# Kernel tuning notes

Hardware: AMD Instinct MI355X
Metric: run time of the kernel (lower is better)

## Reference

```python
import jax, jax.numpy as jnp
import numpy as np

N, E, H, L = 50000, 400000, 100, 2
NF, EF = 16, 8
BN_EPS = 1e-5  # torch BatchNorm1d eps; eval mode with running_mean=0, running_var=1


def setup_inputs() -> dict:
    key = jax.random.key(0)
    ks = jax.random.split(key, 32)
    s = 0.05
    rn = lambda k, shape: jax.random.normal(k, shape, dtype=jnp.float32) * s
    return {
        "x": jax.random.normal(ks[0], (N, NF), dtype=jnp.float32),
        "edge_index": jax.random.randint(ks[1], (2, E), 0, N, dtype=jnp.int32),
        "edge_attr": jax.random.normal(ks[2], (E, EF), dtype=jnp.float32),
        "node_w": rn(ks[3], (NF, H)), "node_b": rn(ks[4], (H,)),
        "edge_w": rn(ks[5], (EF, H)), "edge_b": rn(ks[6], (H,)),
        "conv_w1": rn(ks[7], (L, H, H)), "conv_b1": rn(ks[8], (L, H)),
        "conv_w2": rn(ks[9], (L, H, H)), "conv_b2": rn(ks[10], (L, H)),
        "bn_gamma": jnp.ones((L, H), jnp.float32), "bn_beta": jnp.zeros((L, H), jnp.float32),
        "em_w1": rn(ks[11], (L, 3 * H, H)), "em_b1": rn(ks[12], (L, H)),
        "em_w2": rn(ks[13], (L, H, H)), "em_b2": rn(ks[14], (L, H)),
        "mlp_w1": rn(ks[15], (3 * H, 50)), "mlp_b1": rn(ks[16], (50,)),
        "mlp_w2": rn(ks[17], (50, 25)), "mlp_b2": rn(ks[18], (25,)),
        "mlp_w3": rn(ks[19], (25, 1)), "mlp_b3": rn(ks[20], (1,)),
    }


def reference(x, edge_index, edge_attr, node_w, node_b, edge_w, edge_b,
              conv_w1, conv_b1, conv_w2, conv_b2, bn_gamma, bn_beta,
              em_w1, em_b1, em_w2, em_b2,
              mlp_w1, mlp_b1, mlp_w2, mlp_b2, mlp_w3, mlp_b3):
    src, dst = edge_index[0], edge_index[1]
    h = x @ node_w + node_b            # [N,H]
    e = edge_attr @ edge_w + edge_b    # [E,H]
    bn_inv = 1.0 / jnp.sqrt(1.0 + BN_EPS)
    for i in range(L):
        # GINEConv (eps=0): MLP(x + sum_{j->i} relu(x_j + e_ji))
        msg = jax.nn.relu(h[src] + e)                                  # [E,H]
        agg = jax.ops.segment_sum(msg, dst, num_segments=h.shape[0])   # [N,H]
        z = h + agg
        z = jax.nn.relu(z @ conv_w1[i] + conv_b1[i]) @ conv_w2[i] + conv_b2[i]
        bn = z * (bn_gamma[i] * bn_inv) + bn_beta[i]                   # BN eval (mean 0, var 1)
        h = (h + jax.nn.relu(bn)) * 0.5
        ei = jnp.concatenate([h[src], h[dst], e], axis=-1)             # [E,3H]
        e = e + (jax.nn.relu(ei @ em_w1[i] + em_b1[i]) @ em_w2[i] + em_b2[i]) * 0.5
    xe = jnp.concatenate([h[src], h[dst], e], axis=-1)                 # [E,3H]
    o = jax.nn.relu(xe @ mlp_w1 + mlp_b1)
    o = jax.nn.relu(o @ mlp_w2 + mlp_b2)
    return (o @ mlp_w3 + mlp_b3)[:, 0]                                 # [E]
```

## Files before the change

### kernel.cpp

```cpp
#include <hip/hip_runtime.h>

#define HD 100
#define NF 16
#define EF 8
#define NN 50000
#define NE 400000
#define NT64 6250

typedef __attribute__((ext_vector_type(8))) short bf16x8;
typedef __attribute__((ext_vector_type(4))) float f32x4;

__device__ __forceinline__ float frelu(float v) { return v > 0.f ? v : 0.f; }
__device__ __forceinline__ unsigned short f2bf(float f) {
  unsigned int u = __float_as_uint(f);
  unsigned int r = (u + 0x7FFF + ((u >> 16) & 1)) >> 16;
  return (unsigned short)r;
}
__device__ __forceinline__ int SWZ(int row, int byte) { return byte ^ ((row & 7) << 4); }
__device__ __forceinline__ float4 L4(const float* p) { return *(const float4*)p; }
__device__ __forceinline__ uint2 bf2x4(float4 f, float4 g) {
  uint2 o;
  o.x = (unsigned)f2bf(f.x) | ((unsigned)f2bf(f.y) << 16);
  o.y = (unsigned)f2bf(f.z) | ((unsigned)f2bf(f.w) << 16);
  (void)g;
  return o;
}

__global__ __launch_bounds__(256) void k_pack(const float* __restrict__ W,
    unsigned short* __restrict__ out, int K, int N, int KS, int NT) {
  int t = blockIdx.x * 256 + threadIdx.x;
  if (t >= KS * NT * 64) return;
  int lane = t & 63, nt = (t >> 6) % NT, ks = (t >> 6) / NT;
  int kb = ks * 32 + (lane >> 4) * 8, n = nt * 16 + (lane & 15);
  unsigned short v[8];
  #pragma unroll
  for (int j = 0; j < 8; ++j) {
    int k = kb + j;
    float f = (k < K && n < N) ? W[(size_t)k * N + n] : 0.f;
    v[j] = f2bf(f);
  }
  uint4 o4;
  o4.x = (unsigned)v[0] | ((unsigned)v[1] << 16);
  o4.y = (unsigned)v[2] | ((unsigned)v[3] << 16);
  o4.z = (unsigned)v[4] | ((unsigned)v[5] << 16);
  o4.w = (unsigned)v[6] | ((unsigned)v[7] << 16);
  *(uint4*)&out[(size_t)t * 8] = o4;
}

__global__ __launch_bounds__(256) void k_node_embed(const float* __restrict__ x,
    const float* __restrict__ w, const float* __restrict__ b, float* __restrict__ h) {
  int t = blockIdx.x * 256 + threadIdx.x;
  int n = t / HD, o = t % HD;
  if (n >= NN) return;
  float acc = b[o];
  #pragma unroll
  for (int k = 0; k < NF; ++k) acc = fmaf(x[n * NF + k], w[k * HD + o], acc);
  h[(size_t)n * HD + o] = acc;
}

__global__ __launch_bounds__(256) void k_edge_embed_perm(const float* __restrict__ ea,
    const int* __restrict__ eids, const float* __restrict__ w, const float* __restrict__ b,
    float* __restrict__ e) {
  __shared__ float ws_[EF * HD];
  __shared__ float bs_[HD];
  int tid = threadIdx.x;
  for (int i = tid; i < EF * HD; i += 256) ws_[i] = w[i];
  for (int i = tid; i < HD; i += 256) bs_[i] = b[i];
  __syncthreads();
  long long t = (long long)blockIdx.x * 256 + tid;
  int p = (int)(t / 25), c4 = (int)(t % 25);
  if (p >= NE) return;
  int eid = eids[p];
  const float* ap = ea + (size_t)eid * EF;
  float4 a0 = L4(ap), a1 = L4(ap + 4);
  float av[8] = {a0.x, a0.y, a0.z, a0.w, a1.x, a1.y, a1.z, a1.w};
  int c0 = c4 * 4;
  float o0 = bs_[c0], o1 = bs_[c0 + 1], o2 = bs_[c0 + 2], o3 = bs_[c0 + 3];
  #pragma unroll
  for (int k = 0; k < EF; ++k) {
    const float* wr = &ws_[k * HD + c0];
    o0 = fmaf(av[k], wr[0], o0); o1 = fmaf(av[k], wr[1], o1);
    o2 = fmaf(av[k], wr[2], o2); o3 = fmaf(av[k], wr[3], o3);
  }
  float4 o; o.x = o0; o.y = o1; o.z = o2; o.w = o3;
  ((float4*)e)[(size_t)p * 25 + c4] = o;
}

__global__ __launch_bounds__(256) void k_hist(const int* __restrict__ dst, int* __restrict__ deg) {
  int eid = blockIdx.x * 256 + threadIdx.x;
  if (eid < NE) atomicAdd(&deg[dst[eid]], 1);
}
__global__ __launch_bounds__(256) void k_scan_part(const int* __restrict__ deg, int* __restrict__ part) {
  __shared__ int sm[256];
  int i = blockIdx.x * 256 + threadIdx.x;
  sm[threadIdx.x] = (i < NN) ? deg[i] : 0;
  __syncthreads();
  for (int s = 128; s > 0; s >>= 1) {
    if (threadIdx.x < s) sm[threadIdx.x] += sm[threadIdx.x + s];
    __syncthreads();
  }
  if (threadIdx.x == 0) part[blockIdx.x] = sm[0];
}
__global__ __launch_bounds__(256) void k_scan_top(int* __restrict__ part, int nb) {
  __shared__ int sm[256];
  int v = (threadIdx.x < nb) ? part[threadIdx.x] : 0;
  sm[threadIdx.x] = v;
  __syncthreads();
  for (int off = 1; off < 256; off <<= 1) {
    int t = (threadIdx.x >= (unsigned)off) ? sm[threadIdx.x - off] : 0;
    __syncthreads();
    sm[threadIdx.x] += t;
    __syncthreads();
  }
  if (threadIdx.x < nb) part[threadIdx.x] = sm[threadIdx.x] - v;
}
__global__ __launch_bounds__(256) void k_scan_fill(const int* __restrict__ deg,
    const int* __restrict__ part, int* __restrict__ rowptr) {
  __shared__ int sm[256];
  int i = blockIdx.x * 256 + threadIdx.x;
  int v = (i < NN) ? deg[i] : 0;
  sm[threadIdx.x] = v;
  __syncthreads();
  for (int off = 1; off < 256; off <<= 1) {
    int t = (threadIdx.x >= (unsigned)off) ? sm[threadIdx.x - off] : 0;
    __syncthreads();
    sm[threadIdx.x] += t;
    __syncthreads();
  }
  if (i <= NN) rowptr[i] = part[blockIdx.x] + sm[threadIdx.x] - v;
}
__global__ __launch_bounds__(256) void k_copy(const int* __restrict__ a, int* __restrict__ b) {
  int i = blockIdx.x * 256 + threadIdx.x;
  if (i < NN) b[i] = a[i];
}
__global__ __launch_bounds__(256) void k_fill(const int* __restrict__ dst,
    int* __restrict__ cursor, int* __restrict__ eids) {
  int eid = blockIdx.x * 256 + threadIdx.x;
  if (eid >= NE) return;
  int pos = atomicAdd(&cursor[dst[eid]], 1);
  eids[pos] = eid;
}

__global__ __launch_bounds__(256) void k_gather(const float* __restrict__ h,
    const float* __restrict__ e, const int* __restrict__ rowptr,
    const int* __restrict__ eids, const int* __restrict__ src, float* __restrict__ agg) {
  int slot = threadIdx.x >> 2, sub = threadIdx.x & 3;
  int n = blockIdx.x * 64 + slot;
  if (n >= NN) return;
  int r0 = rowptr[n], r1 = rowptr[n + 1];
  float4 acc[7];
  #pragma unroll
  for (int i = 0; i < 7; ++i) { acc[i].x = 0.f; acc[i].y = 0.f; acc[i].z = 0.f; acc[i].w = 0.f; }
  for (int p = r0; p < r1; ++p) {
    int s = src[eids[p]];
    const float4* hp = (const float4*)&h[(size_t)s * HD];
    const float4* ep = (const float4*)&e[(size_t)p * HD];
    #pragma unroll
    for (int i = 0; i < 7; ++i) {
      int c = sub + i * 4;
      if (c < 25) {
        float4 hv = hp[c], ev = ep[c];
        acc[i].x += frelu(hv.x + ev.x);
        acc[i].y += frelu(hv.y + ev.y);
        acc[i].z += frelu(hv.z + ev.z);
        acc[i].w += frelu(hv.w + ev.w);
      }
    }
  }
  float4* ap = (float4*)&agg[(size_t)n * HD];
  #pragma unroll
  for (int i = 0; i < 7; ++i) {
    int c = sub + i * 4;
    if (c < 25) ap[c] = acc[i];
  }
}

__global__ __launch_bounds__(256) void k_node_update(float* __restrict__ h,
    const float* __restrict__ agg,
    const float* __restrict__ w1, const float* __restrict__ b1,
    const float* __restrict__ w2, const float* __restrict__ b2,
    const float* __restrict__ gamma, const float* __restrict__ beta) {
  __shared__ float zs[64 * 101];
  int tid = threadIdx.x;
  int base = blockIdx.x * 64;
  for (int idx = tid; idx < 64 * HD; idx += 256) {
    int n = idx / HD, k = idx % HD;
    int gn = base + n; int cn = gn < NN ? gn : NN - 1;
    zs[n * 101 + k] = h[(size_t)cn * HD + k] + agg[(size_t)cn * HD + k];
  }
  __syncthreads();
  int el = tid & 63;
  int o0 = __builtin_amdgcn_readfirstlane((tid >> 6) * 25);
  float* row = &zs[el * 101];
  float acc[25];
  #pragma unroll
  for (int j = 0; j < 25; ++j) acc[j] = b1[o0 + j];
  for (int k = 0; k < HD; ++k) {
    float a = row[k];
    const float* wr = &w1[k * HD + o0];
    #pragma unroll
    for (int j = 0; j < 25; ++j) acc[j] = fmaf(a, wr[j], acc[j]);
  }
  __syncthreads();
  #pragma unroll
  for (int j = 0; j < 25; ++j) row[o0 + j] = frelu(acc[j]);
  __syncthreads();
  float acc2[25];
  #pragma unroll
  for (int j = 0; j < 25; ++j) acc2[j] = b2[o0 + j];
  for (int k = 0; k < HD; ++k) {
    float a = row[k];
    const float* wr = &w2[k * HD + o0];
    #pragma unroll
    for (int j = 0; j < 25; ++j) acc2[j] = fmaf(a, wr[j], acc2[j]);
  }
  int gn = base + el;
  if (gn < NN) {
    const float bninv = 0.99999500003749973f;
    #pragma unroll
    for (int j = 0; j < 25; ++j) {
      int o = o0 + j;
      float bn = acc2[j] * (gamma[o] * bninv) + beta[o];
      h[(size_t)gn * HD + o] = (h[(size_t)gn * HD + o] + frelu(bn)) * 0.5f;
    }
  }
}

__global__ __launch_bounds__(512) void k_edge_mfma(
    const float* __restrict__ h, float* __restrict__ e,
    const int* __restrict__ eids, const int* __restrict__ src, const int* __restrict__ dst,
    const unsigned short* __restrict__ w1p, const float* __restrict__ b1,
    const unsigned short* __restrict__ w2p, const float* __restrict__ b2) {
  __shared__ __align__(16) char lds[151040];
  char* W1L = lds;
  char* W2L = lds + 64512;
  char* A1  = lds + 93184;
  char* A2  = lds + 134144;
  int* ss  = (int*)(lds + 150528);
  int* ds_ = (int*)(lds + 150784);
  int tid = threadIdx.x;
  for (int i = tid; i < 4032; i += 512) ((uint4*)W1L)[i] = ((const uint4*)w1p)[i];
  for (int i = tid; i < 1792; i += 512) ((uint4*)W2L)[i] = ((const uint4*)w2p)[i];

  int lane = tid & 63, w = tid >> 6;
  int l15 = lane & 15, lq = lane >> 4;
  int g = w >> 2;
  int arow = (w & 3) * 16 + l15;
  int ntb = g * 4, ntc = g ? 3 : 4;
  f32x4 zero = {0.f, 0.f, 0.f, 0.f};

  for (int tile = blockIdx.x; tile < NT64; tile += gridDim.x) {
    int base = tile * 64;
    if (tid < 64) { int eid = eids[base + tid]; ss[tid] = src[eid]; ds_[tid] = dst[eid]; }
    __syncthreads();
    for (int idx = tid; idx < 64 * 25; idx += 512) {
      int row = idx / 25, c4 = idx % 25;
      float4 f = ((const float4*)e)[(size_t)(base + row) * 25 + c4];
      *(uint2*)(A1 + SWZ(row, row * 640 + 400 + c4 * 8)) = bf2x4(f, f);
    }
    for (int idx = tid; idx < 64 * 25; idx += 512) {
      int row = idx / 25, c4 = idx % 25;
      float4 f = ((const float4*)h)[(size_t)ss[row] * 25 + c4];
      *(uint2*)(A1 + SWZ(row, row * 640 + c4 * 8)) = bf2x4(f, f);
    }
    for (int idx = tid; idx < 64 * 25; idx += 512) {
      int row = idx / 25, c4 = idx % 25;
      float4 f = ((const float4*)h)[(size_t)ds_[row] * 25 + c4];
      *(uint2*)(A1 + SWZ(row, row * 640 + 200 + c4 * 8)) = bf2x4(f, f);
    }
    for (int idx = tid; idx < 64 * 5; idx += 512) {
      int row = idx / 5, j = idx % 5;
      uint2 z; z.x = 0u; z.y = 0u;
      *(uint2*)(A1 + SWZ(row, row * 640 + 600 + j * 8)) = z;
    }
    __syncthreads();
    f32x4 acc[4];
    #pragma unroll
    for (int i = 0; i < 4; ++i) acc[i] = zero;
    #pragma unroll
    for (int ks = 0; ks < 10; ++ks) {
      bf16x8 a = *(const bf16x8*)(A1 + SWZ(arow, arow * 640 + (ks * 32 + lq * 8) * 2));
      #pragma unroll
      for (int i = 0; i < 4; ++i) {
        if (i < ntc) {
          int nt = ntb + i;
          bf16x8 b = (ks < 9)
            ? *(const bf16x8*)(W1L + ks * 7168 + (nt * 64 + lane) * 16)
            : *(const bf16x8*)(w1p + (size_t)9 * 3584 + (nt * 64 + lane) * 8);
          acc[i] = __builtin_amdgcn_mfma_f32_16x16x32_bf16(a, b, acc[i], 0, 0, 0);
        }
      }
    }
    #pragma unroll
    for (int i = 0; i < 4; ++i) {
      if (i < ntc) {
        int o = (ntb + i) * 16 + l15;
        float bias = (o < HD) ? b1[o] : 0.f;
        #pragma unroll
        for (int ii = 0; ii < 4; ++ii) {
          int r = (w & 3) * 16 + lq * 4 + ii;
          float v = acc[i][ii] + bias;
          v = (o < HD) ? frelu(v) : 0.f;
          *(unsigned short*)(A2 + SWZ(r, r * 256 + o * 2)) = f2bf(v);
        }
      }
    }
    for (int idx = tid; idx < 64 * 8; idx += 512) {
      int r = idx / 8, c = idx % 8;
      *(unsigned int*)(A2 + SWZ(r, r * 256 + 224 + c * 4)) = 0;
    }
    __syncthreads();
    f32x4 acc2[4];
    #pragma unroll
    for (int i = 0; i < 4; ++i) acc2[i] = zero;
    #pragma unroll
    for (int ks = 0; ks < 4; ++ks) {
      bf16x8 a = *(const bf16x8*)(A2 + SWZ(arow, arow * 256 + (ks * 32 + lq * 8) * 2));
      #pragma unroll
      for (int i = 0; i < 4; ++i) {
        if (i < ntc) {
          int nt = ntb + i;
          bf16x8 b = *(const bf16x8*)(W2L + ks * 7168 + (nt * 64 + lane) * 16);
          acc2[i] = __builtin_amdgcn_mfma_f32_16x16x32_bf16(a, b, acc2[i], 0, 0, 0);
        }
      }
    }
    #pragma unroll
    for (int i = 0; i < 4; ++i) {
      if (i < ntc) {
        int o = (ntb + i) * 16 + l15;
        if (o < HD) {
          float bias = b2[o];
          #pragma unroll
          for (int ii = 0; ii < 4; ++ii) {
            int r = (w & 3) * 16 + lq * 4 + ii;
            size_t pp = (size_t)(base + r) * HD + o;
            e[pp] = e[pp] + 0.5f * (acc2[i][ii] + bias);
          }
        }
      }
    }
    __syncthreads();
  }
}

__global__ __launch_bounds__(512) void k_edge_final_mfma(
    const float* __restrict__ h, const float* __restrict__ e,
    const int* __restrict__ eids, const int* __restrict__ src, const int* __restrict__ dst,
    const unsigned short* __restrict__ w1p, const float* __restrict__ b1,
    const unsigned short* __restrict__ w2p, const float* __restrict__ b2,
    const unsigned short* __restrict__ wf1p, const float* __restrict__ fb1,
    const float* __restrict__ fw2, const float* __restrict__ fb2,
    const float* __restrict__ fw3, const float* __restrict__ fb3,
    float* __restrict__ out) {
  __shared__ __align__(16) char lds[156500];
  char* W1L = lds;
  char* W2L = lds + 64512;
  char* A1  = lds + 93184;
  char* A2  = lds + 134144;
  float* W2s = (float*)(lds + 150528);
  float* b2s = (float*)(lds + 155528);
  float* W3s = (float*)(lds + 155628);
  float* b3s = (float*)(lds + 155728);
  int* es  = (int*)(lds + 155732);
  int* ss  = (int*)(lds + 155988);
  int* ds_ = (int*)(lds + 156244);
  int tid = threadIdx.x;
  for (int i = tid; i < 4032; i += 512) ((uint4*)W1L)[i] = ((const uint4*)w1p)[i];
  for (int i = tid; i < 1792; i += 512) ((uint4*)W2L)[i] = ((const uint4*)w2p)[i];
  for (int i = tid; i < 1250; i += 512) W2s[i] = fw2[i];
  if (tid < 25) { b2s[tid] = fb2[tid]; W3s[tid] = fw3[tid]; }
  if (tid == 0) b3s[0] = fb3[0];

  int lane = tid & 63, w = tid >> 6;
  int l15 = lane & 15, lq = lane >> 4;
  int g = w >> 2;
  int arow = (w & 3) * 16 + l15;
  int ntb = g * 4, ntc = g ? 3 : 4;
  f32x4 zero = {0.f, 0.f, 0.f, 0.f};

  for (int tile = blockIdx.x; tile < NT64; tile += gridDim.x) {
    int base = tile * 64;
    if (tid < 64) {
      int eid = eids[base + tid];
      es[tid] = eid; ss[tid] = src[eid]; ds_[tid] = dst[eid];
    }
    __syncthreads();
    for (int idx = tid; idx < 64 * 25; idx += 512) {
      int row = idx / 25, c4 = idx % 25;
      float4 f = ((const float4*)e)[(size_t)(base + row) * 25 + c4];
      *(uint2*)(A1 + SWZ(row, row * 640 + 400 + c4 * 8)) = bf2x4(f, f);
    }
    for (int idx = tid; idx < 64 * 25; idx += 512) {
      int row = idx / 25, c4 = idx % 25;
      float4 f = ((const float4*)h)[(size_t)ss[row] * 25 + c4];
      *(uint2*)(A1 + SWZ(row, row * 640 + c4 * 8)) = bf2x4(f, f);
    }
    for (int idx = tid; idx < 64 * 25; idx += 512) {
      int row = idx / 25, c4 = idx % 25;
      float4 f = ((const float4*)h)[(size_t)ds_[row] * 25 + c4];
      *(uint2*)(A1 + SWZ(row, row * 640 + 200 + c4 * 8)) = bf2x4(f, f);
    }
    for (int idx = tid; idx < 64 * 5; idx += 512) {
      int row = idx / 5, j = idx % 5;
      uint2 z; z.x = 0u; z.y = 0u;
      *(uint2*)(A1 + SWZ(row, row * 640 + 600 + j * 8)) = z;
    }
    __syncthreads();
    f32x4 acc[4];
    #pragma unroll
    for (int i = 0; i < 4; ++i) acc[i] = zero;
    #pragma unroll
    for (int ks = 0; ks < 10; ++ks) {
      bf16x8 a = *(const bf16x8*)(A1 + SWZ(arow, arow * 640 + (ks * 32 + lq * 8) * 2));
      #pragma unroll
      for (int i = 0; i < 4; ++i) {
        if (i < ntc) {
          int nt = ntb + i;
          bf16x8 b = (ks < 9)
            ? *(const bf16x8*)(W1L + ks * 7168 + (nt * 64 + lane) * 16)
            : *(const bf16x8*)(w1p + (size_t)9 * 3584 + (nt * 64 + lane) * 8);
          acc[i] = __builtin_amdgcn_mfma_f32_16x16x32_bf16(a, b, acc[i], 0, 0, 0);
        }
      }
    }
    #pragma unroll
    for (int i = 0; i < 4; ++i) {
      if (i < ntc) {
        int o = (ntb + i) * 16 + l15;
        float bias = (o < HD) ? b1[o] : 0.f;
        #pragma unroll
        for (int ii = 0; ii < 4; ++ii) {
          int r = (w & 3) * 16 + lq * 4 + ii;
          float v = acc[i][ii] + bias;
          v = (o < HD) ? frelu(v) : 0.f;
          *(unsigned short*)(A2 + SWZ(r, r * 256 + o * 2)) = f2bf(v);
        }
      }
    }
    for (int idx = tid; idx < 64 * 8; idx += 512) {
      int r = idx / 8, c = idx % 8;
      *(unsigned int*)(A2 + SWZ(r, r * 256 + 224 + c * 4)) = 0;
    }
    __syncthreads();
    f32x4 acc2[4];
    #pragma unroll
    for (int i = 0; i < 4; ++i) acc2[i] = zero;
    #pragma unroll
    for (int ks = 0; ks < 4; ++ks) {
      bf16x8 a = *(const bf16x8*)(A2 + SWZ(arow, arow * 256 + (ks * 32 + lq * 8) * 2));
      #pragma unroll
      for (int i = 0; i < 4; ++i) {
        if (i < ntc) {
          int nt = ntb + i;
          bf16x8 b = *(const bf16x8*)(W2L + ks * 7168 + (nt * 64 + lane) * 16);
          acc2[i] = __builtin_amdgcn_mfma_f32_16x16x32_bf16(a, b, acc2[i], 0, 0, 0);
        }
      }
    }
    #pragma unroll
    for (int i = 0; i < 4; ++i) {
      if (i < ntc) {
        int o = (ntb + i) * 16 + l15;
        if (o < HD) {
          float bias = b2[o];
          #pragma unroll
          for (int ii = 0; ii < 4; ++ii) {
            int r = (w & 3) * 16 + lq * 4 + ii;
            float ne = e[(size_t)(base + r) * HD + o] + 0.5f * (acc2[i][ii] + bias);
            *(unsigned short*)(A1 + SWZ(r, r * 640 + (200 + o) * 2)) = f2bf(ne);
          }
        }
      }
    }
    __syncthreads();
    f32x4 acc3[2];
    acc3[0] = zero; acc3[1] = zero;
    #pragma unroll
    for (int ks = 0; ks < 10; ++ks) {
      bf16x8 a = *(const bf16x8*)(A1 + SWZ(arow, arow * 640 + (ks * 32 + lq * 8) * 2));
      #pragma unroll
      for (int i = 0; i < 2; ++i) {
        int nt = g * 2 + i;
        bf16x8 b = *(const bf16x8*)(wf1p + ((size_t)(ks * 4 + nt) * 64 + lane) * 8);
        acc3[i] = __builtin_amdgcn_mfma_f32_16x16x32_bf16(a, b, acc3[i], 0, 0, 0);
      }
    }
    __syncthreads();
    #pragma unroll
    for (int i = 0; i < 2; ++i) {
      int o = (g * 2 + i) * 16 + l15;
      if (o < 50) {
        float bias = fb1[o];
        #pragma unroll
        for (int ii = 0; ii < 4; ++ii) {
          int r = (w & 3) * 16 + lq * 4 + ii;
          *(float*)(A2 + r * 208 + o * 4) = frelu(acc3[i][ii] + bias);
        }
      }
    }
    __syncthreads();
    {
      int elg = tid >> 3, q8 = tid & 7;
      const float* trow = (const float*)(A2 + elg * 208);
      float s[4];
      {
        int i = 0;
        #pragma unroll
        for (int j0 = 0; j0 < 25; j0 += 8) { if (j0 + q8 < 25) s[i++] = b2s[j0 + q8]; }
      }
      for (int k = 0; k < 50; ++k) {
        float tv = trow[k];
        int i = 0;
        #pragma unroll
        for (int j0 = 0; j0 < 25; j0 += 8) {
          if (j0 + q8 < 25) { s[i] = fmaf(tv, W2s[k * 25 + j0 + q8], s[i]); ++i; }
        }
      }
      float racc = 0.f;
      {
        int i = 0;
        #pragma unroll
        for (int j0 = 0; j0 < 25; j0 += 8) {
          if (j0 + q8 < 25) { racc = fmaf(frelu(s[i]), W3s[j0 + q8], racc); ++i; }
        }
      }
      racc += __shfl_xor(racc, 1, 8);
      racc += __shfl_xor(racc, 2, 8);
      racc += __shfl_xor(racc, 4, 8);
      if (q8 == 0) out[es[elg]] = racc + b3s[0];
    }
    __syncthreads();
  }
}

extern "C" void kernel_launch(void* const* d_in, const int* in_sizes, int n_in,
                              void* d_out, int out_size, void* d_ws, size_t ws_size,
                              hipStream_t stream) {
  (void)in_sizes; (void)n_in; (void)out_size; (void)ws_size;
  const float* x       = (const float*)d_in[0];
  const int*   eidx    = (const int*)  d_in[1];
  const float* eattr   = (const float*)d_in[2];
  const float* node_w  = (const float*)d_in[3];
  const float* node_b  = (const float*)d_in[4];
  const float* edge_w  = (const float*)d_in[5];
  const float* edge_b  = (const float*)d_in[6];
  const float* conv_w1 = (const float*)d_in[7];
  const float* conv_b1 = (const float*)d_in[8];
  const float* conv_w2 = (const float*)d_in[9];
  const float* conv_b2 = (const float*)d_in[10];
  const float* bn_g    = (const float*)d_in[11];
  const float* bn_b    = (const float*)d_in[12];
  const float* em_w1   = (const float*)d_in[13];
  const float* em_b1   = (const float*)d_in[14];
  const float* em_w2   = (const float*)d_in[15];
  const float* em_b2   = (const float*)d_in[16];
  const float* mlp_w1  = (const float*)d_in[17];
  const float* mlp_b1  = (const float*)d_in[18];
  const float* mlp_w2  = (const float*)d_in[19];
  const float* mlp_b2  = (const float*)d_in[20];
  const float* mlp_w3  = (const float*)d_in[21];
  const float* mlp_b3  = (const float*)d_in[22];

  const int* src = eidx;
  const int* dst = eidx + NE;

  char* ws = (char*)d_ws;
  float* h    = (float*)(ws);
  float* agg  = (float*)(ws + 20000000);
  float* e    = (float*)(ws + 40000000);
  unsigned short* w1p  = (unsigned short*)(ws + 200000000);
  unsigned short* w2p  = (unsigned short*)(ws + 200071680);
  unsigned short* wf1p = (unsigned short*)(ws + 200100352);
  int* rowptr = (int*)(ws + 200141312);
  int* cursor = (int*)(ws + 200341504);
  int* eids   = (int*)(ws + 200541504);
  int* part   = (int*)(ws + 202141504);

  const int SCAN_NB = (NN + 256) / 256;
  hipMemsetAsync(cursor, 0, (size_t)NN * 4, stream);
  k_hist<<<(NE + 255) / 256, 256, 0, stream>>>(dst, cursor);
  k_scan_part<<<SCAN_NB, 256, 0, stream>>>(cursor, part);
  k_scan_top<<<1, 256, 0, stream>>>(part, SCAN_NB);
  k_scan_fill<<<SCAN_NB, 256, 0, stream>>>(cursor, part, rowptr);
  k_copy<<<SCAN_NB, 256, 0, stream>>>(rowptr, cursor);
  k_fill<<<(NE + 255) / 256, 256, 0, stream>>>(dst, cursor, eids);

  k_node_embed<<<(NN * HD + 255) / 256, 256, 0, stream>>>(x, node_w, node_b, h);
  {
    long long th = (long long)NE * 25;
    k_edge_embed_perm<<<(unsigned)((th + 255) / 256), 256, 0, stream>>>(eattr, eids, edge_w, edge_b, e);
  }

  k_pack<<<(10 * 4 * 64 + 255) / 256, 256, 0, stream>>>(mlp_w1, wf1p, 300, 50, 10, 4);

  for (int i = 0; i < 2; ++i) {
    k_gather<<<(NN + 63) / 64, 256, 0, stream>>>(h, e, rowptr, eids, src, agg);
    k_node_update<<<(NN + 63) / 64, 256, 0, stream>>>(
        h, agg, conv_w1 + i * HD * HD, conv_b1 + i * HD,
        conv_w2 + i * HD * HD, conv_b2 + i * HD, bn_g + i * HD, bn_b + i * HD);
    k_pack<<<(10 * 7 * 64 + 255) / 256, 256, 0, stream>>>(em_w1 + i * 30000, w1p, 300, 100, 10, 7);
    k_pack<<<(4 * 7 * 64 + 255) / 256, 256, 0, stream>>>(em_w2 + i * 10000,  w2p, 100, 100, 4, 7);
    if (i == 0) {
      k_edge_mfma<<<256, 512, 0, stream>>>(
          h, e, eids, src, dst, w1p, em_b1, w2p, em_b2);
    } else {
      k_edge_final_mfma<<<256, 512, 0, stream>>>(
          h, e, eids, src, dst, w1p, em_b1 + HD, w2p, em_b2 + HD,
          wf1p, mlp_b1, mlp_w2, mlp_b2, mlp_w3, mlp_b3, (float*)d_out);
    }
  }
}
```

Baseline: 885.1 us.

## Double-buffer edge tile staging to overlap gathers with MFMA compute

Both edge kernels now gather the next tile's h[src], h[dst] and e rows into a second LDS buffer while the current tile is being multiplied. This hides gather latency and removes a barrier per tile. To make room, W2 and the last two K-slices of W1 are now read from global memory instead of LDS, which adds global and L2 traffic inside the MFMA loops. In the final kernel, one barrier after the third GEMM is removed because A2 no longer aliases the buffer being read.

```diff
diff --git a/kernel.cpp b/kernel.cpp
--- a/kernel.cpp
+++ b/kernel.cpp
@@ -18,11 +18,10 @@
 }
 __device__ __forceinline__ int SWZ(int row, int byte) { return byte ^ ((row & 7) << 4); }
 __device__ __forceinline__ float4 L4(const float* p) { return *(const float4*)p; }
-__device__ __forceinline__ uint2 bf2x4(float4 f, float4 g) {
+__device__ __forceinline__ uint2 pk4(float4 f) {
   uint2 o;
   o.x = (unsigned)f2bf(f.x) | ((unsigned)f2bf(f.y) << 16);
   o.y = (unsigned)f2bf(f.z) | ((unsigned)f2bf(f.w) << 16);
-  (void)g;
   return o;
 }
 
@@ -226,21 +225,47 @@
   }
 }
 
+__device__ __forceinline__ void stage_tile(char* A1b, int tb, int tid,
+    const float* __restrict__ h, const float* __restrict__ e,
+    const int* __restrict__ eids, const int* __restrict__ src, const int* __restrict__ dst) {
+  int nbase = tb * 64;
+  for (int idx = tid; idx < 1600; idx += 512) {
+    int row = idx / 25, c4 = idx % 25;
+    float4 f = ((const float4*)e)[(size_t)(nbase + row) * 25 + c4];
+    *(uint2*)(A1b + SWZ(row, row * 640 + 400 + c4 * 8)) = pk4(f);
+  }
+  for (int idx = tid; idx < 1600; idx += 512) {
+    int row = idx / 25, c4 = idx % 25;
+    int s = src[eids[nbase + row]];
+    float4 f = ((const float4*)h)[(size_t)s * 25 + c4];
+    *(uint2*)(A1b + SWZ(row, row * 640 + c4 * 8)) = pk4(f);
+  }
+  for (int idx = tid; idx < 1600; idx += 512) {
+    int row = idx / 25, c4 = idx % 25;
+    int d = dst[eids[nbase + row]];
+    float4 f = ((const float4*)h)[(size_t)d * 25 + c4];
+    *(uint2*)(A1b + SWZ(row, row * 640 + 200 + c4 * 8)) = pk4(f);
+  }
+  if (tid < 320) {
+    int row = tid / 5, j = tid % 5;
+    uint2 z; z.x = 0u; z.y = 0u;
+    *(uint2*)(A1b + SWZ(row, row * 640 + 600 + j * 8)) = z;
+  }
+}
+
 __global__ __launch_bounds__(512) void k_edge_mfma(
     const float* __restrict__ h, float* __restrict__ e,
     const int* __restrict__ eids, const int* __restrict__ src, const int* __restrict__ dst,
     const unsigned short* __restrict__ w1p, const float* __restrict__ b1,
     const unsigned short* __restrict__ w2p, const float* __restrict__ b2) {
-  __shared__ __align__(16) char lds[151040];
+  __shared__ __align__(16) char lds[155648];
   char* W1L = lds;
-  char* W2L = lds + 64512;
-  char* A1  = lds + 93184;
-  char* A2  = lds + 134144;
-  int* ss  = (int*)(lds + 150528);
-  int* ds_ = (int*)(lds + 150784);
+  char* A1q = lds + 57344;
+  char* A2  = lds + 139264;
   int tid = threadIdx.x;
-  for (int i = tid; i < 4032; i += 512) ((uint4*)W1L)[i] = ((const uint4*)w1p)[i];
-  for (int i = tid; i < 1792; i += 512) ((uint4*)W2L)[i] = ((const uint4*)w2p)[i];
+  for (int i = tid; i < 3584; i += 512) ((uint4*)W1L)[i] = ((const uint4*)w1p)[i];
+  if (blockIdx.x < NT64) stage_tile(A1q, blockIdx.x, tid, h, e, eids, src, dst);
+  __syncthreads();
 
   int lane = tid & 63, w = tid >> 6;
   int l15 = lane & 15, lq = lane >> 4;
@@ -248,32 +273,14 @@
   int arow = (w & 3) * 16 + l15;
   int ntb = g * 4, ntc = g ? 3 : 4;
   f32x4 zero = {0.f, 0.f, 0.f, 0.f};
+  int cb = 0;
 
   for (int tile = blockIdx.x; tile < NT64; tile += gridDim.x) {
     int base = tile * 64;
-    if (tid < 64) { int eid = eids[base + tid]; ss[tid] = src[eid]; ds_[tid] = dst[eid]; }
-    __syncthreads();
-    for (int idx = tid; idx < 64 * 25; idx += 512) {
-      int row = idx / 25, c4 = idx % 25;
-      float4 f = ((const float4*)e)[(size_t)(base + row) * 25 + c4];
-      *(uint2*)(A1 + SWZ(row, row * 640 + 400 + c4 * 8)) = bf2x4(f, f);
-    }
-    for (int idx = tid; idx < 64 * 25; idx += 512) {
-      int row = idx / 25, c4 = idx % 25;
-      float4 f = ((const float4*)h)[(size_t)ss[row] * 25 + c4];
-      *(uint2*)(A1 + SWZ(row, row * 640 + c4 * 8)) = bf2x4(f, f);
-    }
-    for (int idx = tid; idx < 64 * 25; idx += 512) {
-      int row = idx / 25, c4 = idx % 25;
-      float4 f = ((const float4*)h)[(size_t)ds_[row] * 25 + c4];
-      *(uint2*)(A1 + SWZ(row, row * 640 + 200 + c4 * 8)) = bf2x4(f, f);
-    }
-    for (int idx = tid; idx < 64 * 5; idx += 512) {
-      int row = idx / 5, j = idx % 5;
-      uint2 z; z.x = 0u; z.y = 0u;
-      *(uint2*)(A1 + SWZ(row, row * 640 + 600 + j * 8)) = z;
-    }
-    __syncthreads();
+    char* A1 = A1q + cb * 40960;
+    int nxt = tile + gridDim.x;
+    if (nxt < NT64) stage_tile(A1q + (cb ^ 1) * 40960, nxt, tid, h, e, eids, src, dst);
+
     f32x4 acc[4];
     #pragma unroll
     for (int i = 0; i < 4; ++i) acc[i] = zero;
@@ -284,9 +291,9 @@
       for (int i = 0; i < 4; ++i) {
         if (i < ntc) {
           int nt = ntb + i;
-          bf16x8 b = (ks < 9)
+          bf16x8 b = (ks < 8)
             ? *(const bf16x8*)(W1L + ks * 7168 + (nt * 64 + lane) * 16)
-            : *(const bf16x8*)(w1p + (size_t)9 * 3584 + (nt * 64 + lane) * 8);
+            : *(const bf16x8*)(w1p + (size_t)ks * 3584 + (nt * 64 + lane) * 8);
           acc[i] = __builtin_amdgcn_mfma_f32_16x16x32_bf16(a, b, acc[i], 0, 0, 0);
         }
       }
@@ -305,10 +312,8 @@
         }
       }
     }
-    for (int idx = tid; idx < 64 * 8; idx += 512) {
-      int r = idx / 8, c = idx % 8;
-      *(unsigned int*)(A2 + SWZ(r, r * 256 + 224 + c * 4)) = 0;
-    }
+    { int r = tid / 8, c = tid % 8;
+      *(unsigned int*)(A2 + SWZ(r, r * 256 + 224 + c * 4)) = 0; }
     __syncthreads();
     f32x4 acc2[4];
     #pragma unroll
@@ -320,7 +325,7 @@
       for (int i = 0; i < 4; ++i) {
         if (i < ntc) {
           int nt = ntb + i;
-          bf16x8 b = *(const bf16x8*)(W2L + ks * 7168 + (nt * 64 + lane) * 16);
+          bf16x8 b = *(const bf16x8*)(w2p + ((size_t)(ks * 7 + nt) * 64 + lane) * 8);
           acc2[i] = __builtin_amdgcn_mfma_f32_16x16x32_bf16(a, b, acc2[i], 0, 0, 0);
         }
       }
@@ -341,6 +346,7 @@
       }
     }
     __syncthreads();
+    cb ^= 1;
   }
 }
 
@@ -353,24 +359,21 @@
     const float* __restrict__ fw2, const float* __restrict__ fb2,
     const float* __restrict__ fw3, const float* __restrict__ fb3,
     float* __restrict__ out) {
-  __shared__ __align__(16) char lds[156500];
+  __shared__ __align__(16) char lds[160856];
   char* W1L = lds;
-  char* W2L = lds + 64512;
-  char* A1  = lds + 93184;
-  char* A2  = lds + 134144;
-  float* W2s = (float*)(lds + 150528);
-  float* b2s = (float*)(lds + 155528);
-  float* W3s = (float*)(lds + 155628);
-  float* b3s = (float*)(lds + 155728);
-  int* es  = (int*)(lds + 155732);
-  int* ss  = (int*)(lds + 155988);
-  int* ds_ = (int*)(lds + 156244);
+  char* A1q = lds + 57344;
+  char* A2  = lds + 139264;
+  float* W2s = (float*)(lds + 155648);
+  float* b2s = (float*)(lds + 160648);
+  float* W3s = (float*)(lds + 160748);
+  float* b3s = (float*)(lds + 160848);
   int tid = threadIdx.x;
-  for (int i = tid; i < 4032; i += 512) ((uint4*)W1L)[i] = ((const uint4*)w1p)[i];
-  for (int i = tid; i < 1792; i += 512) ((uint4*)W2L)[i] = ((const uint4*)w2p)[i];
+  for (int i = tid; i < 3584; i += 512) ((uint4*)W1L)[i] = ((const uint4*)w1p)[i];
   for (int i = tid; i < 1250; i += 512) W2s[i] = fw2[i];
   if (tid < 25) { b2s[tid] = fb2[tid]; W3s[tid] = fw3[tid]; }
   if (tid == 0) b3s[0] = fb3[0];
+  if (blockIdx.x < NT64) stage_tile(A1q, blockIdx.x, tid, h, e, eids, src, dst);
+  __syncthreads();
 
   int lane = tid & 63, w = tid >> 6;
   int l15 = lane & 15, lq = lane >> 4;
@@ -378,35 +381,14 @@
   int arow = (w & 3) * 16 + l15;
   int ntb = g * 4, ntc = g ? 3 : 4;
   f32x4 zero = {0.f, 0.f, 0.f, 0.f};
+  int cb = 0;
 
   for (int tile = blockIdx.x; tile < NT64; tile += gridDim.x) {
     int base = tile * 64;
-    if (tid < 64) {
-      int eid = eids[base + tid];
-      es[tid] = eid; ss[tid] = src[eid]; ds_[tid] = dst[eid];
-    }
-    __syncthreads();
-    for (int idx = tid; idx < 64 * 25; idx += 512) {
-      int row = idx / 25, c4 = idx % 25;
-      float4 f = ((const float4*)e)[(size_t)(base + row) * 25 + c4];
-      *(uint2*)(A1 + SWZ(row, row * 640 + 400 + c4 * 8)) = bf2x4(f, f);
-    }
-    for (int idx = tid; idx < 64 * 25; idx += 512) {
-      int row = idx / 25, c4 = idx % 25;
-      float4 f = ((const float4*)h)[(size_t)ss[row] * 25 + c4];
-      *(uint2*)(A1 + SWZ(row, row * 640 + c4 * 8)) = bf2x4(f, f);
-    }
-    for (int idx = tid; idx < 64 * 25; idx += 512) {
-      int row = idx / 25, c4 = idx % 25;
-      float4 f = ((const float4*)h)[(size_t)ds_[row] * 25 + c4];
-      *(uint2*)(A1 + SWZ(row, row * 640 + 200 + c4 * 8)) = bf2x4(f, f);
-    }
-    for (int idx = tid; idx < 64 * 5; idx += 512) {
-      int row = idx / 5, j = idx % 5;
-      uint2 z; z.x = 0u; z.y = 0u;
-      *(uint2*)(A1 + SWZ(row, row * 640 + 600 + j * 8)) = z;
-    }
-    __syncthreads();
+    char* A1 = A1q + cb * 40960;
+    int nxt = tile + gridDim.x;
+    if (nxt < NT64) stage_tile(A1q + (cb ^ 1) * 40960, nxt, tid, h, e, eids, src, dst);
+
     f32x4 acc[4];
     #pragma unroll
     for (int i = 0; i < 4; ++i) acc[i] = zero;
@@ -417,9 +399,9 @@
       for (int i = 0; i < 4; ++i) {
         if (i < ntc) {
           int nt = ntb + i;
-          bf16x8 b = (ks < 9)
+          bf16x8 b = (ks < 8)
             ? *(const bf16x8*)(W1L + ks * 7168 + (nt * 64 + lane) * 16)
-            : *(const bf16x8*)(w1p + (size_t)9 * 3584 + (nt * 64 + lane) * 8);
+            : *(const bf16x8*)(w1p + (size_t)ks * 3584 + (nt * 64 + lane) * 8);
           acc[i] = __builtin_amdgcn_mfma_f32_16x16x32_bf16(a, b, acc[i], 0, 0, 0);
         }
       }
@@ -438,10 +420,8 @@
         }
       }
     }
-    for (int idx = tid; idx < 64 * 8; idx += 512) {
-      int r = idx / 8, c = idx % 8;
-      *(unsigned int*)(A2 + SWZ(r, r * 256 + 224 + c * 4)) = 0;
-    }
+    { int r = tid / 8, c = tid % 8;
+      *(unsigned int*)(A2 + SWZ(r, r * 256 + 224 + c * 4)) = 0; }
     __syncthreads();
     f32x4 acc2[4];
     #pragma unroll
@@ -453,7 +433,7 @@
       for (int i = 0; i < 4; ++i) {
         if (i < ntc) {
           int nt = ntb + i;
-          bf16x8 b = *(const bf16x8*)(W2L + ks * 7168 + (nt * 64 + lane) * 16);
+          bf16x8 b = *(const bf16x8*)(w2p + ((size_t)(ks * 7 + nt) * 64 + lane) * 8);
           acc2[i] = __builtin_amdgcn_mfma_f32_16x16x32_bf16(a, b, acc2[i], 0, 0, 0);
         }
       }
@@ -486,7 +466,6 @@
         acc3[i] = __builtin_amdgcn_mfma_f32_16x16x32_bf16(a, b, acc3[i], 0, 0, 0);
       }
     }
-    __syncthreads();
     #pragma unroll
     for (int i = 0; i < 2; ++i) {
       int o = (g * 2 + i) * 16 + l15;
@@ -528,9 +507,10 @@
       racc += __shfl_xor(racc, 1, 8);
       racc += __shfl_xor(racc, 2, 8);
       racc += __shfl_xor(racc, 4, 8);
-      if (q8 == 0) out[es[elg]] = racc + b3s[0];
-    }
-    __syncthreads();
+      if (q8 == 0) out[eids[base + elg]] = racc + b3s[0];
+    }
+    __syncthreads();
+    cb ^= 1;
   }
 }
 
```

Measured after the change: 1.323 ms. +49.5%, slower.

## Drop LDS weight staging in edge MFMA kernels and double grid size

Applied to the files above, without the earlier changes.

Weight fragments for the edge MLP MFMAs are now read straight from global memory (expected to hit L1/L2) rather than staged into LDS once per block. This cuts LDS use per block from about 151KB to about 58-63KB, so two 512-thread blocks can share a CU, and the grid goes from 256 to 512 blocks. Occupancy rises and the per-block weight preload goes away, but every MFMA now issues a global load for its B operand, which may add latency and cache pressure.

```diff
diff --git a/kernel.cpp b/kernel.cpp
--- a/kernel.cpp
+++ b/kernel.cpp
@@ -18,11 +18,10 @@
 }
 __device__ __forceinline__ int SWZ(int row, int byte) { return byte ^ ((row & 7) << 4); }
 __device__ __forceinline__ float4 L4(const float* p) { return *(const float4*)p; }
-__device__ __forceinline__ uint2 bf2x4(float4 f, float4 g) {
+__device__ __forceinline__ uint2 pk4(float4 f) {
   uint2 o;
   o.x = (unsigned)f2bf(f.x) | ((unsigned)f2bf(f.y) << 16);
   o.y = (unsigned)f2bf(f.z) | ((unsigned)f2bf(f.w) << 16);
-  (void)g;
   return o;
 }
 
@@ -231,16 +230,12 @@
     const int* __restrict__ eids, const int* __restrict__ src, const int* __restrict__ dst,
     const unsigned short* __restrict__ w1p, const float* __restrict__ b1,
     const unsigned short* __restrict__ w2p, const float* __restrict__ b2) {
-  __shared__ __align__(16) char lds[151040];
-  char* W1L = lds;
-  char* W2L = lds + 64512;
-  char* A1  = lds + 93184;
-  char* A2  = lds + 134144;
-  int* ss  = (int*)(lds + 150528);
-  int* ds_ = (int*)(lds + 150784);
+  __shared__ __align__(16) char lds[57856];
+  char* A1 = lds;
+  char* A2 = lds + 40960;
+  int* ss  = (int*)(lds + 57344);
+  int* ds_ = (int*)(lds + 57600);
   int tid = threadIdx.x;
-  for (int i = tid; i < 4032; i += 512) ((uint4*)W1L)[i] = ((const uint4*)w1p)[i];
-  for (int i = tid; i < 1792; i += 512) ((uint4*)W2L)[i] = ((const uint4*)w2p)[i];
 
   int lane = tid & 63, w = tid >> 6;
   int l15 = lane & 15, lq = lane >> 4;
@@ -256,17 +251,17 @@
     for (int idx = tid; idx < 64 * 25; idx += 512) {
       int row = idx / 25, c4 = idx % 25;
       float4 f = ((const float4*)e)[(size_t)(base + row) * 25 + c4];
-      *(uint2*)(A1 + SWZ(row, row * 640 + 400 + c4 * 8)) = bf2x4(f, f);
+      *(uint2*)(A1 + SWZ(row, row * 640 + 400 + c4 * 8)) = pk4(f);
     }
     for (int idx = tid; idx < 64 * 25; idx += 512) {
       int row = idx / 25, c4 = idx % 25;
       float4 f = ((const float4*)h)[(size_t)ss[row] * 25 + c4];
-      *(uint2*)(A1 + SWZ(row, row * 640 + c4 * 8)) = bf2x4(f, f);
+      *(uint2*)(A1 + SWZ(row, row * 640 + c4 * 8)) = pk4(f);
     }
     for (int idx = tid; idx < 64 * 25; idx += 512) {
       int row = idx / 25, c4 = idx % 25;
       float4 f = ((const float4*)h)[(size_t)ds_[row] * 25 + c4];
-      *(uint2*)(A1 + SWZ(row, row * 640 + 200 + c4 * 8)) = bf2x4(f, f);
+      *(uint2*)(A1 + SWZ(row, row * 640 + 200 + c4 * 8)) = pk4(f);
     }
     for (int idx = tid; idx < 64 * 5; idx += 512) {
       int row = idx / 5, j = idx % 5;
@@ -284,9 +279,7 @@
       for (int i = 0; i < 4; ++i) {
         if (i < ntc) {
           int nt = ntb + i;
-          bf16x8 b = (ks < 9)
-            ? *(const bf16x8*)(W1L + ks * 7168 + (nt * 64 + lane) * 16)
-            : *(const bf16x8*)(w1p + (size_t)9 * 3584 + (nt * 64 + lane) * 8);
+          bf16x8 b = *(const bf16x8*)(w1p + ((size_t)(ks * 7 + nt) * 64 + lane) * 8);
           acc[i] = __builtin_amdgcn_mfma_f32_16x16x32_bf16(a, b, acc[i], 0, 0, 0);
         }
       }
@@ -305,10 +298,8 @@
         }
       }
     }
-    for (int idx = tid; idx < 64 * 8; idx += 512) {
-      int r = idx / 8, c = idx % 8;
-      *(unsigned int*)(A2 + SWZ(r, r * 256 + 224 + c * 4)) = 0;
-    }
+    { int r = tid / 8, c = tid % 8;
+      *(unsigned int*)(A2 + SWZ(r, r * 256 + 224 + c * 4)) = 0; }
     __syncthreads();
     f32x4 acc2[4];
     #pragma unroll
@@ -320,7 +311,7 @@
       for (int i = 0; i < 4; ++i) {
         if (i < ntc) {
           int nt = ntb + i;
-          bf16x8 b = *(const bf16x8*)(W2L + ks * 7168 + (nt * 64 + lane) * 16);
+          bf16x8 b = *(const bf16x8*)(w2p + ((size_t)(ks * 7 + nt) * 64 + lane) * 8);
           acc2[i] = __builtin_amdgcn_mfma_f32_16x16x32_bf16(a, b, acc2[i], 0, 0, 0);
         }
       }
@@ -353,21 +344,17 @@
     const float* __restrict__ fw2, const float* __restrict__ fb2,
     const float* __restrict__ fw3, const float* __restrict__ fb3,
     float* __restrict__ out) {
-  __shared__ __align__(16) char lds[156500];
-  char* W1L = lds;
-  char* W2L = lds + 64512;
-  char* A1  = lds + 93184;
-  char* A2  = lds + 134144;
-  float* W2s = (float*)(lds + 150528);
-  float* b2s = (float*)(lds + 155528);
-  float* W3s = (float*)(lds + 155628);
-  float* b3s = (float*)(lds + 155728);
-  int* es  = (int*)(lds + 155732);
-  int* ss  = (int*)(lds + 155988);
-  int* ds_ = (int*)(lds + 156244);
+  __shared__ __align__(16) char lds[63320];
+  char* A1 = lds;
+  char* A2 = lds + 40960;
+  float* W2s = (float*)(lds + 57344);
+  float* b2s = (float*)(lds + 62344);
+  float* W3s = (float*)(lds + 62444);
+  float* b3s = (float*)(lds + 62544);
+  int* es  = (int*)(lds + 62548);
+  int* ss  = (int*)(lds + 62804);
+  int* ds_ = (int*)(lds + 63060);
   int tid = threadIdx.x;
-  for (int i = tid; i < 4032; i += 512) ((uint4*)W1L)[i] = ((const uint4*)w1p)[i];
-  for (int i = tid; i < 1792; i += 512) ((uint4*)W2L)[i] = ((const uint4*)w2p)[i];
   for (int i = tid; i < 1250; i += 512) W2s[i] = fw2[i];
   if (tid < 25) { b2s[tid] = fb2[tid]; W3s[tid] = fw3[tid]; }
   if (tid == 0) b3s[0] = fb3[0];
@@ -389,17 +376,17 @@
     for (int idx = tid; idx < 64 * 25; idx += 512) {
       int row = idx / 25, c4 = idx % 25;
       float4 f = ((const float4*)e)[(size_t)(base + row) * 25 + c4];
-      *(uint2*)(A1 + SWZ(row, row * 640 + 400 + c4 * 8)) = bf2x4(f, f);
+      *(uint2*)(A1 + SWZ(row, row * 640 + 400 + c4 * 8)) = pk4(f);
     }
     for (int idx = tid; idx < 64 * 25; idx += 512) {
       int row = idx / 25, c4 = idx % 25;
       float4 f = ((const float4*)h)[(size_t)ss[row] * 25 + c4];
-      *(uint2*)(A1 + SWZ(row, row * 640 + c4 * 8)) = bf2x4(f, f);
+      *(uint2*)(A1 + SWZ(row, row * 640 + c4 * 8)) = pk4(f);
     }
     for (int idx = tid; idx < 64 * 25; idx += 512) {
       int row = idx / 25, c4 = idx % 25;
       float4 f = ((const float4*)h)[(size_t)ds_[row] * 25 + c4];
-      *(uint2*)(A1 + SWZ(row, row * 640 + 200 + c4 * 8)) = bf2x4(f, f);
+      *(uint2*)(A1 + SWZ(row, row * 640 + 200 + c4 * 8)) = pk4(f);
     }
     for (int idx = tid; idx < 64 * 5; idx += 512) {
       int row = idx / 5, j = idx % 5;
@@ -417,9 +404,7 @@
       for (int i = 0; i < 4; ++i) {
         if (i < ntc) {
           int nt = ntb + i;
-          bf16x8 b = (ks < 9)
-            ? *(const bf16x8*)(W1L + ks * 7168 + (nt * 64 + lane) * 16)
-            : *(const bf16x8*)(w1p + (size_t)9 * 3584 + (nt * 64 + lane) * 8);
+          bf16x8 b = *(const bf16x8*)(w1p + ((size_t)(ks * 7 + nt) * 64 + lane) * 8);
           acc[i] = __builtin_amdgcn_mfma_f32_16x16x32_bf16(a, b, acc[i], 0, 0, 0);
         }
       }
@@ -438,10 +423,8 @@
         }
       }
     }
-    for (int idx = tid; idx < 64 * 8; idx += 512) {
-      int r = idx / 8, c = idx % 8;
-      *(unsigned int*)(A2 + SWZ(r, r * 256 + 224 + c * 4)) = 0;
-    }
+    { int r = tid / 8, c = tid % 8;
+      *(unsigned int*)(A2 + SWZ(r, r * 256 + 224 + c * 4)) = 0; }
     __syncthreads();
     f32x4 acc2[4];
     #pragma unroll
@@ -453,7 +436,7 @@
       for (int i = 0; i < 4; ++i) {
         if (i < ntc) {
           int nt = ntb + i;
-          bf16x8 b = *(const bf16x8*)(W2L + ks * 7168 + (nt * 64 + lane) * 16);
+          bf16x8 b = *(const bf16x8*)(w2p + ((size_t)(ks * 7 + nt) * 64 + lane) * 8);
           acc2[i] = __builtin_amdgcn_mfma_f32_16x16x32_bf16(a, b, acc2[i], 0, 0, 0);
         }
       }
@@ -602,10 +585,10 @@
     k_pack<<<(10 * 7 * 64 + 255) / 256, 256, 0, stream>>>(em_w1 + i * 30000, w1p, 300, 100, 10, 7);
     k_pack<<<(4 * 7 * 64 + 255) / 256, 256, 0, stream>>>(em_w2 + i * 10000,  w2p, 100, 100, 4, 7);
     if (i == 0) {
-      k_edge_mfma<<<256, 512, 0, stream>>>(
+      k_edge_mfma<<<512, 512, 0, stream>>>(
           h, e, eids, src, dst, w1p, em_b1, w2p, em_b2);
     } else {
-      k_edge_final_mfma<<<256, 512, 0, stream>>>(
+      k_edge_final_mfma<<<512, 512, 0, stream>>>(
           h, e, eids, src, dst, w1p, em_b1 + HD, w2p, em_b2 + HD,
           wf1p, mlp_b1, mlp_w2, mlp_b2, mlp_w3, mlp_b3, (float*)d_out);
     }
```

After: 1.700 ms. 92.0% more time.
